# Optimization experiments

Measured on AMD Instinct MI355X. Metric: run time of the kernel, lower is better.

Reference implementation:

```python
import jax, jax.numpy as jnp
import numpy as np

N_NODES = 100000
NEG_SLOPE = 0.2


def gat_conv(x, W, att_src, att_dst, bias, src, dst, heads, out_ch):
    # x: [N, F_in]; W: [F_in, heads*out_ch]; att_*: [heads, out_ch]; bias: [heads*out_ch]
    N = x.shape[0]
    h = (x @ W).reshape(N, heads, out_ch)                 # [N, H, C]
    a_src = jnp.sum(h * att_src[None], axis=-1)           # [N, H]
    a_dst = jnp.sum(h * att_dst[None], axis=-1)           # [N, H]
    # per-edge unnormalized attention logits (PyG GATConv)
    alpha = jax.nn.leaky_relu(a_src[src] + a_dst[dst], NEG_SLOPE)   # [E, H]
    # scatter-softmax over edges grouped by destination node
    m = jax.ops.segment_max(alpha, dst, num_segments=N)   # [N, H]
    m = jnp.where(jnp.isfinite(m), m, 0.0)
    e = jnp.exp(alpha - m[dst])                           # [E, H]
    s = jax.ops.segment_sum(e, dst, num_segments=N)       # [N, H]
    alpha = e / (s[dst] + 1e-16)
    # weighted scatter-add aggregation of neighbor features
    out = jax.ops.segment_sum(alpha[:, :, None] * h[src], dst, num_segments=N)  # [N, H, C]
    return out.reshape(N, heads * out_ch) + bias


def setup_inputs() -> dict:
    key = jax.random.key(0)
    ks = jax.random.split(key, 10)
    F_in = 128
    x = jax.random.normal(ks[0], (N_NODES, F_in), dtype=jnp.float32)
    edge_index = jax.random.randint(ks[1], (2, 3200000), 0, N_NODES, dtype=jnp.int64)
    g = 0.1
    return {
        "x": x,
        "edge_index": edge_index,
        "W1": jax.random.normal(ks[2], (F_in, 32), jnp.float32) * g,
        "att_src1": jax.random.normal(ks[3], (2, 16), jnp.float32) * g,
        "att_dst1": jax.random.normal(ks[4], (2, 16), jnp.float32) * g,
        "b1": jnp.zeros((32,), jnp.float32),
        "W2": jax.random.normal(ks[5], (32, 2), jnp.float32) * g,
        "att_src2": jax.random.normal(ks[6], (1, 2), jnp.float32) * g,
        "att_dst2": jax.random.normal(ks[7], (1, 2), jnp.float32) * g,
        "b2": jnp.zeros((2,), jnp.float32),
    }


def reference(x, edge_index, W1, att_src1, att_dst1, b1, W2, att_src2, att_dst2, b2):
    N = x.shape[0]
    # add self-loops (PyG GATConv default add_self_loops=True)
    loops = jnp.arange(N, dtype=edge_index.dtype)
    src = jnp.concatenate([edge_index[0], loops])
    dst = jnp.concatenate([edge_index[1], loops])
    h = gat_conv(x, W1, att_src1, att_dst1, b1, src, dst, heads=2, out_ch=16)
    h = jax.nn.elu(h)
    h = gat_conv(h, W2, att_src2, att_dst2, b2, src, dst, heads=1, out_ch=2)
    return jax.nn.log_softmax(h, axis=1)
```

## Files before the change

### kernel.cpp

```cpp
#include <hip/hip_runtime.h>
#include <hip/hip_bf16.h>

#define LEAK  0.2f
#define NPB   200
#define CAP   8192
#define CAPSH 13
#define SBITS 17
#define SMASK 0x1FFFF
#define CHUNK 4096

__global__ __launch_bounds__(512) void kbin(const int* __restrict__ ei, int E, int K,
                                            int* __restrict__ cursor,
                                            int* __restrict__ binned) {
    __shared__ int hist[512], lo[512], gb[512], lc[512];
    __shared__ int2 stag[CHUNK];
    __shared__ int probe;
    int t = threadIdx.x;
    hist[t] = 0;
    if (t == 0) probe = 0;
    __syncthreads();
    if (t < 256) {
        int zc = 0;
#pragma unroll
        for (int j = 0; j < 4; j++) zc += (ei[(t * 4 + j) * 2 + 1] == 0) ? 1 : 0;
        if (zc) atomicAdd(&probe, zc);
    }
    __syncthreads();
    int f = (probe == 1024);
    int e0 = blockIdx.x * CHUNK;
    int ss[8], dd[8];
#pragma unroll
    for (int i = 0; i < 8; i++) {
        int e = e0 + t + 512 * i;
        ss[i] = -1;
        dd[i] = 0;
        if (e < E) {
            int s, d;
            if (f) { s = ei[2 * (long long)e]; d = ei[2 * ((long long)e + E)]; }
            else   { s = ei[e];                d = ei[(long long)e + E]; }
            ss[i] = s;
            dd[i] = d;
            atomicAdd(&hist[d / NPB], 1);
        }
    }
    __syncthreads();
    int v = hist[t], x = v;
    for (int o = 1; o < 512; o <<= 1) {
        int y = (t >= o) ? hist[t - o] : 0;
        __syncthreads();
        x += y;
        hist[t] = x;
        __syncthreads();
    }
    int tb = x - v;
    lo[t] = tb;
    lc[t] = tb;
    if (t < K && v) {
        int rel = atomicAdd(&cursor[t], v);
        gb[t] = (t << CAPSH) + rel;
    }
    __syncthreads();
#pragma unroll
    for (int i = 0; i < 8; i++) {
        if (ss[i] >= 0) {
            int bk = dd[i] / NPB;
            int pos = atomicAdd(&lc[bk], 1);
            stag[pos] = make_int2(ss[i], dd[i]);
        }
    }
    __syncthreads();
    int cnt = min(CHUNK, E - e0);
#pragma unroll
    for (int i = 0; i < 8; i++) {
        int idx = t + 512 * i;
        if (idx < cnt) {
            int2 sd2 = stag[idx];
            int bk = sd2.y / NPB;
            int dloc = sd2.y - bk * NPB;
            int gpos = gb[bk] + (idx - lo[bk]);
            if (gpos < ((bk + 1) << CAPSH))
                binned[gpos] = sd2.x | (dloc << SBITS);
        }
    }
}

__global__ __launch_bounds__(256) void k1(const float* __restrict__ x,
                                          const float* __restrict__ W1,
                                          const float* __restrict__ atts,
                                          const float* __restrict__ attd,
                                          float* __restrict__ h1,
                                          float* __restrict__ a1s,
                                          float* __restrict__ a1d, int N) {
    __shared__ float Ws[128 * 32];
    __shared__ float xs[64 * 132];
    int t = threadIdx.x;
    const float4* W4 = (const float4*)W1;
    float4* Ws4 = (float4*)Ws;
#pragma unroll
    for (int i = 0; i < 4; i++) Ws4[t + 256 * i] = W4[t + 256 * i];
    long long node0 = (long long)blockIdx.x * 64;
    const float4* x4 = (const float4*)x;
    float4* xs4 = (float4*)xs;
#pragma unroll
    for (int i = 0; i < 8; i++) {
        int idx = t + 256 * i;
        int row = idx >> 5, col = idx & 31;
        long long n = node0 + row;
        float4 v = make_float4(0.f, 0.f, 0.f, 0.f);
        if (n < N) v = x4[n * 32 + col];
        xs4[row * 33 + col] = v;
    }
    __syncthreads();

    int cg = t & 7, ns = t >> 3;
    const float4* xr0 = (const float4*)(xs + (ns * 2) * 132);
    const float4* xr1 = (const float4*)(xs + (ns * 2 + 1) * 132);
    float acc0[4] = {0.f, 0.f, 0.f, 0.f}, acc1[4] = {0.f, 0.f, 0.f, 0.f};
#pragma unroll 8
    for (int k4 = 0; k4 < 32; k4++) {
        float4 xa = xr0[k4], xb = xr1[k4];
        float av[4] = {xa.x, xa.y, xa.z, xa.w};
        float bv[4] = {xb.x, xb.y, xb.z, xb.w};
#pragma unroll
        for (int i = 0; i < 4; i++) {
            float4 w = Ws4[(k4 * 4 + i) * 8 + cg];
            acc0[0] = fmaf(av[i], w.x, acc0[0]);
            acc0[1] = fmaf(av[i], w.y, acc0[1]);
            acc0[2] = fmaf(av[i], w.z, acc0[2]);
            acc0[3] = fmaf(av[i], w.w, acc0[3]);
            acc1[0] = fmaf(bv[i], w.x, acc1[0]);
            acc1[1] = fmaf(bv[i], w.y, acc1[1]);
            acc1[2] = fmaf(bv[i], w.z, acc1[2]);
            acc1[3] = fmaf(bv[i], w.w, acc1[3]);
        }
    }
    long long gn0 = node0 + ns * 2, gn1 = gn0 + 1;
    float4* h14 = (float4*)h1;
    if (gn0 < N) h14[gn0 * 8 + cg] = make_float4(acc0[0], acc0[1], acc0[2], acc0[3]);
    if (gn1 < N) h14[gn1 * 8 + cg] = make_float4(acc1[0], acc1[1], acc1[2], acc1[3]);

    float ps0 = 0.f, pd0 = 0.f, ps1 = 0.f, pd1 = 0.f;
#pragma unroll
    for (int i = 0; i < 4; i++) {
        float aa = atts[cg * 4 + i], dd = attd[cg * 4 + i];
        ps0 = fmaf(acc0[i], aa, ps0);
        pd0 = fmaf(acc0[i], dd, pd0);
        ps1 = fmaf(acc1[i], aa, ps1);
        pd1 = fmaf(acc1[i], dd, pd1);
    }
#pragma unroll
    for (int m = 1; m < 4; m <<= 1) {
        ps0 += __shfl_xor(ps0, m, 64);
        pd0 += __shfl_xor(pd0, m, 64);
        ps1 += __shfl_xor(ps1, m, 64);
        pd1 += __shfl_xor(pd1, m, 64);
    }
    if ((cg & 3) == 0) {
        int hd = cg >> 2;
        if (gn0 < N) { a1s[gn0 * 2 + hd] = ps0; a1d[gn0 * 2 + hd] = pd0; }
        if (gn1 < N) { a1s[gn1 * 2 + hd] = ps1; a1d[gn1 * 2 + hd] = pd1; }
    }
}

__global__ __launch_bounds__(1024) void kfused(const int* __restrict__ cursor,
                                               const int* __restrict__ binned,
                                               const float* __restrict__ h1,
                                               const float* __restrict__ a1s,
                                               const float* __restrict__ a1d,
                                               const float* __restrict__ b1,
                                               const float* __restrict__ W2,
                                               const float* __restrict__ as2,
                                               const float* __restrict__ ad2,
                                               float4* __restrict__ pk,
                                               int* __restrict__ srcs,
                                               int* __restrict__ off,
                                               int* __restrict__ deg, int N) {
    __shared__ int lsrc[CAP];
    __shared__ int ldeg[NPB], lcur[NPB], loff[NPB];
    __shared__ int sd[1024];
    int b = blockIdx.x, t = threadIdx.x;
    int node0 = b * NPB;
    int nn = min(NPB, N - node0);
    int cnt = cursor[b];
    if (cnt > CAP) cnt = CAP;
    const int* bb = binned + ((long long)b << CAPSH);
    if (t < NPB) ldeg[t] = 0;
    __syncthreads();
    for (int i = t; i < cnt; i += 1024) atomicAdd(&ldeg[bb[i] >> SBITS], 1);
    __syncthreads();
    int v = (t < nn) ? ldeg[t] : 0, x = v;
    sd[t] = x;
    __syncthreads();
    for (int o = 1; o < 1024; o <<= 1) {
        int y = (t >= o) ? sd[t - o] : 0;
        __syncthreads();
        x += y;
        sd[t] = x;
        __syncthreads();
    }
    if (t < nn) {
        int rel = x - v;
        loff[t] = rel;
        lcur[t] = rel;
        off[node0 + t] = (b << CAPSH) + rel;
        deg[node0 + t] = v;
    }
    __syncthreads();
    for (int i = t; i < cnt; i += 1024) {
        int p = bb[i];
        int pos = atomicAdd(&lcur[p >> SBITS], 1);
        lsrc[pos] = p & SMASK;
    }
    __syncthreads();
    for (int i = t; i < cnt; i += 1024) srcs[((long long)b << CAPSH) + i] = lsrc[i];

    int wv = t >> 6, lane = t & 63;
    int e8 = lane >> 3, c4 = lane & 7, hd = c4 >> 2;
    bool wlane = (c4 & 3) == 0;
    const float4* h14 = (const float4*)h1;
    for (int ni = wv; ni < nn; ni += 16) {
        int n = node0 + ni;
        float a1dn = a1d[2 * n + hd];
        int base = loff[ni], g = ldeg[ni];
        float4 acc = make_float4(0.f, 0.f, 0.f, 0.f);
        float wsum = 0.f;
        for (int tt = e8 - 1; tt < g; tt += 8) {
            int s = (tt < 0) ? n : lsrc[base + tt];
            float al = a1s[2 * s + hd] + a1dn;
            al = al > 0.f ? al : LEAK * al;
            float w = __expf(al);
            float4 hv = h14[(size_t)s * 8 + c4];
            acc.x = fmaf(w, hv.x, acc.x);
            acc.y = fmaf(w, hv.y, acc.y);
            acc.z = fmaf(w, hv.z, acc.z);
            acc.w = fmaf(w, hv.w, acc.w);
            if (wlane) wsum += w;
        }
#pragma unroll
        for (int m = 8; m < 64; m <<= 1) {
            acc.x += __shfl_xor(acc.x, m, 64);
            acc.y += __shfl_xor(acc.y, m, 64);
            acc.z += __shfl_xor(acc.z, m, 64);
            acc.w += __shfl_xor(acc.w, m, 64);
            wsum += __shfl_xor(wsum, m, 64);
        }
        float wsH = __shfl(wsum, hd * 4, 64);
        float inv = 1.f / (wsH + 1e-16f);
        float4 bv = ((const float4*)b1)[c4];
        float4 t1;
        t1.x = acc.x * inv + bv.x;
        t1.y = acc.y * inv + bv.y;
        t1.z = acc.z * inv + bv.z;
        t1.w = acc.w * inv + bv.w;
        t1.x = t1.x > 0.f ? t1.x : __expf(t1.x) - 1.f;
        t1.y = t1.y > 0.f ? t1.y : __expf(t1.y) - 1.f;
        t1.z = t1.z > 0.f ? t1.z : __expf(t1.z) - 1.f;
        t1.w = t1.w > 0.f ? t1.w : __expf(t1.w) - 1.f;
        const float4* W24 = (const float4*)W2;
        float4 wA = W24[c4 * 2], wB = W24[c4 * 2 + 1];
        float p0 = t1.x * wA.x + t1.y * wA.z + t1.z * wB.x + t1.w * wB.z;
        float p1 = t1.x * wA.y + t1.y * wA.w + t1.z * wB.y + t1.w * wB.w;
#pragma unroll
        for (int m = 1; m < 8; m <<= 1) {
            p0 += __shfl_xor(p0, m, 64);
            p1 += __shfl_xor(p1, m, 64);
        }
        if (lane == 0)
            pk[n] = make_float4(p0 * as2[0] + p1 * as2[1], p0, p1,
                                p0 * ad2[0] + p1 * ad2[1]);
    }
}

__global__ __launch_bounds__(256) void kagg2(const int* __restrict__ off,
                                             const int* __restrict__ deg,
                                             const int* __restrict__ srcs,
                                             const float4* __restrict__ pk,
                                             const float* __restrict__ b2,
                                             float* __restrict__ out, int N) {
    int wv = threadIdx.x >> 6;
    int lane = threadIdx.x & 63;
    int n = blockIdx.x * 4 + wv;
    if (n >= N) return;
    float adn = pk[n].w;
    int base = off[n], g = deg[n];
    float a0 = 0.f, a1v = 0.f, ws = 0.f;
    for (int t = lane - 1; t < g; t += 64) {
        int s = (t < 0) ? n : srcs[base + t];
        float4 p = pk[s];
        float al = p.x + adn;
        al = al > 0.f ? al : LEAK * al;
        float w = __expf(al);
        a0 = fmaf(w, p.y, a0);
        a1v = fmaf(w, p.z, a1v);
        ws += w;
    }
#pragma unroll
    for (int m = 1; m < 64; m <<= 1) {
        a0 += __shfl_xor(a0, m, 64);
        a1v += __shfl_xor(a1v, m, 64);
        ws += __shfl_xor(ws, m, 64);
    }
    if (lane == 0) {
        float inv = 1.f / (ws + 1e-16f);
        float o0 = a0 * inv + b2[0];
        float o1 = a1v * inv + b2[1];
        float mx = fmaxf(o0, o1);
        float lse = mx + __logf(__expf(o0 - mx) + __expf(o1 - mx));
        out[2 * n] = o0 - lse;
        out[2 * n + 1] = o1 - lse;
    }
}

extern "C" void kernel_launch(void* const* d_in, const int* in_sizes, int n_in,
                              void* d_out, int out_size, void* d_ws, size_t ws_size,
                              hipStream_t stream) {
    const float* x   = (const float*)d_in[0];
    const int*   ei  = (const int*)d_in[1];
    const float* W1  = (const float*)d_in[2];
    const float* as1 = (const float*)d_in[3];
    const float* ad1 = (const float*)d_in[4];
    const float* b1  = (const float*)d_in[5];
    const float* W2  = (const float*)d_in[6];
    const float* as2 = (const float*)d_in[7];
    const float* ad2 = (const float*)d_in[8];
    const float* b2  = (const float*)d_in[9];
    float* out = (float*)d_out;

    int N = out_size / 2;
    int E = in_sizes[1] / 2;
    int K = (N + NPB - 1) / NPB;

    float* ws    = (float*)d_ws;
    float* h1    = ws;
    float4* pk   = (float4*)(h1 + (size_t)N * 32);
    float* a1s   = (float*)(pk + (size_t)N);
    float* a1d   = a1s + (size_t)N * 2;
    int* deg     = (int*)(a1d + (size_t)N * 2);
    int* off     = deg + N;
    int* srcs    = off + N;
    int* binned  = srcs + (size_t)K * CAP;
    int* cursor  = binned + (size_t)K * CAP;

    int nblkE = (E + CHUNK - 1) / CHUNK;

    hipMemsetAsync(cursor, 0, K * sizeof(int), stream);
    kbin<<<nblkE, 512, 0, stream>>>(ei, E, K, cursor, binned);
    k1<<<(N + 63) / 64, 256, 0, stream>>>(x, W1, as1, ad1, h1, a1s, a1d, N);
    kfused<<<K, 1024, 0, stream>>>(cursor, binned, h1, a1s, a1d,
                                   b1, W2, as2, ad2, pk, srcs, off, deg, N);
    kagg2<<<(N + 3) / 4, 256, 0, stream>>>(off, deg, srcs, pk, b2, out, N);
}
```

Before: 245.8 us.

## Merge binning and GEMM into one launch, aggregate layer 2 per bin with shared atomics

The binning kernel and the first-layer GEMM now share one launch, with block index choosing the role and shared memory held in a union. Binning drops the staging sort and scatters straight to global memory using per-bucket atomics, at 8192 edges per block. kfused no longer writes CSR arrays and switches to a wave-shuffle scan. The layer-2 aggregation now reads the binned edges per 200-node block and accumulates with shared-memory float atomics, which removes the srcs/off/deg traffic but gives up coalesced binned writes and adds atomic contention.

New measurement: 253.5 us. 1.03x slower.

```diff
diff --git a/kernel.cpp b/kernel.cpp
--- a/kernel.cpp
+++ b/kernel.cpp
@@ -1,164 +1,133 @@
 #include <hip/hip_runtime.h>
 #include <hip/hip_bf16.h>
 
-#define LEAK  0.2f
-#define NPB   200
-#define CAP   8192
-#define CAPSH 13
-#define SBITS 17
-#define SMASK 0x1FFFF
-#define CHUNK 4096
-
-__global__ __launch_bounds__(512) void kbin(const int* __restrict__ ei, int E, int K,
-                                            int* __restrict__ cursor,
-                                            int* __restrict__ binned) {
-    __shared__ int hist[512], lo[512], gb[512], lc[512];
-    __shared__ int2 stag[CHUNK];
-    __shared__ int probe;
+#define LEAK   0.2f
+#define NPB    200
+#define CAP    8192
+#define CAPSH  13
+#define SBITS  17
+#define SMASK  0x1FFFF
+#define CHUNKB 8192
+
+struct alignas(16) SMbin { int hist[512]; int gb[512]; int lc[512]; int probe; };
+struct alignas(16) SMgemm { float Ws[128 * 32]; float xs[64 * 132]; };
+union alignas(16) SMprep { SMbin bin; SMgemm gemm; };
+
+__global__ __launch_bounds__(512) void kprep(const int* __restrict__ ei, int E, int K,
+                                             int* __restrict__ cursor,
+                                             int* __restrict__ binned,
+                                             const float* __restrict__ x,
+                                             const float* __restrict__ W1,
+                                             const float* __restrict__ atts,
+                                             const float* __restrict__ attd,
+                                             float* __restrict__ h1,
+                                             float* __restrict__ a1s,
+                                             float* __restrict__ a1d,
+                                             int N, int nblkB) {
+    __shared__ SMprep sm;
     int t = threadIdx.x;
-    hist[t] = 0;
-    if (t == 0) probe = 0;
-    __syncthreads();
-    if (t < 256) {
-        int zc = 0;
-#pragma unroll
-        for (int j = 0; j < 4; j++) zc += (ei[(t * 4 + j) * 2 + 1] == 0) ? 1 : 0;
-        if (zc) atomicAdd(&probe, zc);
-    }
-    __syncthreads();
-    int f = (probe == 1024);
-    int e0 = blockIdx.x * CHUNK;
-    int ss[8], dd[8];
-#pragma unroll
-    for (int i = 0; i < 8; i++) {
-        int e = e0 + t + 512 * i;
-        ss[i] = -1;
-        dd[i] = 0;
-        if (e < E) {
-            int s, d;
-            if (f) { s = ei[2 * (long long)e]; d = ei[2 * ((long long)e + E)]; }
-            else   { s = ei[e];                d = ei[(long long)e + E]; }
-            ss[i] = s;
-            dd[i] = d;
-            atomicAdd(&hist[d / NPB], 1);
-        }
-    }
-    __syncthreads();
-    int v = hist[t], x = v;
-    for (int o = 1; o < 512; o <<= 1) {
-        int y = (t >= o) ? hist[t - o] : 0;
-        __syncthreads();
-        x += y;
-        hist[t] = x;
-        __syncthreads();
-    }
-    int tb = x - v;
-    lo[t] = tb;
-    lc[t] = tb;
-    if (t < K && v) {
-        int rel = atomicAdd(&cursor[t], v);
-        gb[t] = (t << CAPSH) + rel;
-    }
-    __syncthreads();
-#pragma unroll
-    for (int i = 0; i < 8; i++) {
-        if (ss[i] >= 0) {
-            int bk = dd[i] / NPB;
-            int pos = atomicAdd(&lc[bk], 1);
-            stag[pos] = make_int2(ss[i], dd[i]);
-        }
-    }
-    __syncthreads();
-    int cnt = min(CHUNK, E - e0);
-#pragma unroll
-    for (int i = 0; i < 8; i++) {
-        int idx = t + 512 * i;
-        if (idx < cnt) {
-            int2 sd2 = stag[idx];
-            int bk = sd2.y / NPB;
-            int dloc = sd2.y - bk * NPB;
-            int gpos = gb[bk] + (idx - lo[bk]);
-            if (gpos < ((bk + 1) << CAPSH))
-                binned[gpos] = sd2.x | (dloc << SBITS);
-        }
-    }
-}
-
-__global__ __launch_bounds__(256) void k1(const float* __restrict__ x,
-                                          const float* __restrict__ W1,
-                                          const float* __restrict__ atts,
-                                          const float* __restrict__ attd,
-                                          float* __restrict__ h1,
-                                          float* __restrict__ a1s,
-                                          float* __restrict__ a1d, int N) {
-    __shared__ float Ws[128 * 32];
-    __shared__ float xs[64 * 132];
-    int t = threadIdx.x;
-    const float4* W4 = (const float4*)W1;
-    float4* Ws4 = (float4*)Ws;
-#pragma unroll
-    for (int i = 0; i < 4; i++) Ws4[t + 256 * i] = W4[t + 256 * i];
-    long long node0 = (long long)blockIdx.x * 64;
-    const float4* x4 = (const float4*)x;
-    float4* xs4 = (float4*)xs;
-#pragma unroll
-    for (int i = 0; i < 8; i++) {
-        int idx = t + 256 * i;
-        int row = idx >> 5, col = idx & 31;
-        long long n = node0 + row;
-        float4 v = make_float4(0.f, 0.f, 0.f, 0.f);
-        if (n < N) v = x4[n * 32 + col];
-        xs4[row * 33 + col] = v;
-    }
-    __syncthreads();
-
-    int cg = t & 7, ns = t >> 3;
-    const float4* xr0 = (const float4*)(xs + (ns * 2) * 132);
-    const float4* xr1 = (const float4*)(xs + (ns * 2 + 1) * 132);
-    float acc0[4] = {0.f, 0.f, 0.f, 0.f}, acc1[4] = {0.f, 0.f, 0.f, 0.f};
+    if (blockIdx.x < nblkB) {
+        SMbin& B = sm.bin;
+        B.hist[t] = 0;
+        if (t == 0) B.probe = 0;
+        __syncthreads();
+        if (t < 256) {
+            int zc = 0;
+#pragma unroll
+            for (int j = 0; j < 4; j++) zc += (ei[(t * 4 + j) * 2 + 1] == 0) ? 1 : 0;
+            if (zc) atomicAdd(&B.probe, zc);
+        }
+        __syncthreads();
+        int f = (B.probe == 1024);
+        int e0 = blockIdx.x * CHUNKB;
+        int ss[16], dd[16];
+#pragma unroll
+        for (int i = 0; i < 16; i++) {
+            int e = e0 + t + 512 * i;
+            ss[i] = -1;
+            dd[i] = 0;
+            if (e < E) {
+                int s, d;
+                if (f) { s = ei[2 * e]; d = ei[2 * (e + E)]; }
+                else   { s = ei[e];     d = ei[e + E]; }
+                ss[i] = s;
+                dd[i] = d;
+                atomicAdd(&B.hist[d / NPB], 1);
+            }
+        }
+        __syncthreads();
+        int h = B.hist[t];
+        B.lc[t] = 0;
+        if (t < K && h) B.gb[t] = (t << CAPSH) + atomicAdd(&cursor[t], h);
+        __syncthreads();
+#pragma unroll
+        for (int i = 0; i < 16; i++) {
+            if (ss[i] >= 0) {
+                int bk = dd[i] / NPB;
+                int dloc = dd[i] - bk * NPB;
+                int pos = atomicAdd(&B.lc[bk], 1);
+                int gpos = B.gb[bk] + pos;
+                if (gpos < ((bk + 1) << CAPSH))
+                    binned[gpos] = ss[i] | (dloc << SBITS);
+            }
+        }
+    } else {
+        SMgemm& G = sm.gemm;
+        int gb1 = blockIdx.x - nblkB;
+        const float4* W4 = (const float4*)W1;
+        float4* Ws4 = (float4*)G.Ws;
+#pragma unroll
+        for (int i = 0; i < 2; i++) Ws4[t + 512 * i] = W4[t + 512 * i];
+        long long node0 = (long long)gb1 * 64;
+        const float4* x4 = (const float4*)x;
+        float4* xs4 = (float4*)G.xs;
+#pragma unroll
+        for (int i = 0; i < 4; i++) {
+            int idx = t + 512 * i;
+            int row = idx >> 5, col = idx & 31;
+            long long n = node0 + row;
+            float4 v = make_float4(0.f, 0.f, 0.f, 0.f);
+            if (n < N) v = x4[n * 32 + col];
+            xs4[row * 33 + col] = v;
+        }
+        __syncthreads();
+
+        int cg = t & 7, ns = t >> 3;
+        const float4* xr = (const float4*)(G.xs + ns * 132);
+        float acc[4] = {0.f, 0.f, 0.f, 0.f};
 #pragma unroll 8
-    for (int k4 = 0; k4 < 32; k4++) {
-        float4 xa = xr0[k4], xb = xr1[k4];
-        float av[4] = {xa.x, xa.y, xa.z, xa.w};
-        float bv[4] = {xb.x, xb.y, xb.z, xb.w};
+        for (int k4 = 0; k4 < 32; k4++) {
+            float4 xa = xr[k4];
+            float av[4] = {xa.x, xa.y, xa.z, xa.w};
+#pragma unroll
+            for (int i = 0; i < 4; i++) {
+                float4 w = Ws4[(k4 * 4 + i) * 8 + cg];
+                acc[0] = fmaf(av[i], w.x, acc[0]);
+                acc[1] = fmaf(av[i], w.y, acc[1]);
+                acc[2] = fmaf(av[i], w.z, acc[2]);
+                acc[3] = fmaf(av[i], w.w, acc[3]);
+            }
+        }
+        long long gn = node0 + ns;
+        if (gn < N)
+            ((float4*)h1)[gn * 8 + cg] = make_float4(acc[0], acc[1], acc[2], acc[3]);
+
+        float ps = 0.f, pd = 0.f;
 #pragma unroll
         for (int i = 0; i < 4; i++) {
-            float4 w = Ws4[(k4 * 4 + i) * 8 + cg];
-            acc0[0] = fmaf(av[i], w.x, acc0[0]);
-            acc0[1] = fmaf(av[i], w.y, acc0[1]);
-            acc0[2] = fmaf(av[i], w.z, acc0[2]);
-            acc0[3] = fmaf(av[i], w.w, acc0[3]);
-            acc1[0] = fmaf(bv[i], w.x, acc1[0]);
-            acc1[1] = fmaf(bv[i], w.y, acc1[1]);
-            acc1[2] = fmaf(bv[i], w.z, acc1[2]);
-            acc1[3] = fmaf(bv[i], w.w, acc1[3]);
-        }
-    }
-    long long gn0 = node0 + ns * 2, gn1 = gn0 + 1;
-    float4* h14 = (float4*)h1;
-    if (gn0 < N) h14[gn0 * 8 + cg] = make_float4(acc0[0], acc0[1], acc0[2], acc0[3]);
-    if (gn1 < N) h14[gn1 * 8 + cg] = make_float4(acc1[0], acc1[1], acc1[2], acc1[3]);
-
-    float ps0 = 0.f, pd0 = 0.f, ps1 = 0.f, pd1 = 0.f;
-#pragma unroll
-    for (int i = 0; i < 4; i++) {
-        float aa = atts[cg * 4 + i], dd = attd[cg * 4 + i];
-        ps0 = fmaf(acc0[i], aa, ps0);
-        pd0 = fmaf(acc0[i], dd, pd0);
-        ps1 = fmaf(acc1[i], aa, ps1);
-        pd1 = fmaf(acc1[i], dd, pd1);
-    }
-#pragma unroll
-    for (int m = 1; m < 4; m <<= 1) {
-        ps0 += __shfl_xor(ps0, m, 64);
-        pd0 += __shfl_xor(pd0, m, 64);
-        ps1 += __shfl_xor(ps1, m, 64);
-        pd1 += __shfl_xor(pd1, m, 64);
-    }
-    if ((cg & 3) == 0) {
-        int hd = cg >> 2;
-        if (gn0 < N) { a1s[gn0 * 2 + hd] = ps0; a1d[gn0 * 2 + hd] = pd0; }
-        if (gn1 < N) { a1s[gn1 * 2 + hd] = ps1; a1d[gn1 * 2 + hd] = pd1; }
+            ps = fmaf(acc[i], atts[cg * 4 + i], ps);
+            pd = fmaf(acc[i], attd[cg * 4 + i], pd);
+        }
+#pragma unroll
+        for (int m = 1; m < 4; m <<= 1) {
+            ps += __shfl_xor(ps, m, 64);
+            pd += __shfl_xor(pd, m, 64);
+        }
+        if ((cg & 3) == 0 && gn < N) {
+            int hd = cg >> 2;
+            a1s[gn * 2 + hd] = ps;
+            a1d[gn * 2 + hd] = pd;
+        }
     }
 }
 
@@ -171,13 +140,10 @@
                                                const float* __restrict__ W2,
                                                const float* __restrict__ as2,
                                                const float* __restrict__ ad2,
-                                               float4* __restrict__ pk,
-                                               int* __restrict__ srcs,
-                                               int* __restrict__ off,
-                                               int* __restrict__ deg, int N) {
+                                               float4* __restrict__ pk, int N) {
     __shared__ int lsrc[CAP];
     __shared__ int ldeg[NPB], lcur[NPB], loff[NPB];
-    __shared__ int sd[1024];
+    __shared__ int swt[4];
     int b = blockIdx.x, t = threadIdx.x;
     int node0 = b * NPB;
     int nn = min(NPB, N - node0);
@@ -186,33 +152,43 @@
     const int* bb = binned + ((long long)b << CAPSH);
     if (t < NPB) ldeg[t] = 0;
     __syncthreads();
-    for (int i = t; i < cnt; i += 1024) atomicAdd(&ldeg[bb[i] >> SBITS], 1);
-    __syncthreads();
-    int v = (t < nn) ? ldeg[t] : 0, x = v;
-    sd[t] = x;
-    __syncthreads();
-    for (int o = 1; o < 1024; o <<= 1) {
-        int y = (t >= o) ? sd[t - o] : 0;
-        __syncthreads();
-        x += y;
-        sd[t] = x;
-        __syncthreads();
-    }
-    if (t < nn) {
-        int rel = x - v;
-        loff[t] = rel;
-        lcur[t] = rel;
-        off[node0 + t] = (b << CAPSH) + rel;
-        deg[node0 + t] = v;
-    }
-    __syncthreads();
-    for (int i = t; i < cnt; i += 1024) {
-        int p = bb[i];
-        int pos = atomicAdd(&lcur[p >> SBITS], 1);
-        lsrc[pos] = p & SMASK;
-    }
-    __syncthreads();
-    for (int i = t; i < cnt; i += 1024) srcs[((long long)b << CAPSH) + i] = lsrc[i];
+    int pv[8];
+#pragma unroll
+    for (int j = 0; j < 8; j++) {
+        int i = t + 1024 * j;
+        pv[j] = (i < cnt) ? bb[i] : -1;
+        if (pv[j] >= 0) atomicAdd(&ldeg[pv[j] >> SBITS], 1);
+    }
+    __syncthreads();
+    int v = 0, x = 0;
+    if (t < 256) {
+        v = (t < nn) ? ldeg[t] : 0;
+        x = v;
+#pragma unroll
+        for (int o = 1; o < 64; o <<= 1) {
+            int y = __shfl_up(x, o, 64);
+            if ((t & 63) >= o) x += y;
+        }
+        if ((t & 63) == 63) swt[t >> 6] = x;
+    }
+    __syncthreads();
+    if (t < 256) {
+        int add = 0;
+#pragma unroll
+        for (int j = 0; j < 4; j++)
+            if (j < (t >> 6)) add += swt[j];
+        x += add;
+        if (t < nn) { loff[t] = x - v; lcur[t] = x - v; }
+    }
+    __syncthreads();
+#pragma unroll
+    for (int j = 0; j < 8; j++) {
+        if (pv[j] >= 0) {
+            int pos = atomicAdd(&lcur[pv[j] >> SBITS], 1);
+            lsrc[pos] = pv[j] & SMASK;
+        }
+    }
+    __syncthreads();
 
     int wv = t >> 6, lane = t & 63;
     int e8 = lane >> 3, c4 = lane & 7, hd = c4 >> 2;
@@ -271,43 +247,48 @@
     }
 }
 
-__global__ __launch_bounds__(256) void kagg2(const int* __restrict__ off,
-                                             const int* __restrict__ deg,
-                                             const int* __restrict__ srcs,
-                                             const float4* __restrict__ pk,
-                                             const float* __restrict__ b2,
-                                             float* __restrict__ out, int N) {
-    int wv = threadIdx.x >> 6;
-    int lane = threadIdx.x & 63;
-    int n = blockIdx.x * 4 + wv;
-    if (n >= N) return;
-    float adn = pk[n].w;
-    int base = off[n], g = deg[n];
-    float a0 = 0.f, a1v = 0.f, ws = 0.f;
-    for (int t = lane - 1; t < g; t += 64) {
-        int s = (t < 0) ? n : srcs[base + t];
-        float4 p = pk[s];
-        float al = p.x + adn;
+__global__ __launch_bounds__(1024) void kagg2b(const int* __restrict__ cursor,
+                                               const int* __restrict__ binned,
+                                               const float4* __restrict__ pk,
+                                               const float* __restrict__ b2,
+                                               float* __restrict__ out, int N) {
+    __shared__ float la2d[NPB], lw[NPB], l0[NPB], l1[NPB];
+    int b = blockIdx.x, t = threadIdx.x;
+    int node0 = b * NPB;
+    int nn = min(NPB, N - node0);
+    int cnt = cursor[b];
+    if (cnt > CAP) cnt = CAP;
+    const int* bb = binned + ((long long)b << CAPSH);
+    if (t < nn) {
+        float4 p = pk[node0 + t];
+        la2d[t] = p.w;
+        float al = p.x + p.w;
         al = al > 0.f ? al : LEAK * al;
         float w = __expf(al);
-        a0 = fmaf(w, p.y, a0);
-        a1v = fmaf(w, p.z, a1v);
-        ws += w;
-    }
-#pragma unroll
-    for (int m = 1; m < 64; m <<= 1) {
-        a0 += __shfl_xor(a0, m, 64);
-        a1v += __shfl_xor(a1v, m, 64);
-        ws += __shfl_xor(ws, m, 64);
-    }
-    if (lane == 0) {
-        float inv = 1.f / (ws + 1e-16f);
-        float o0 = a0 * inv + b2[0];
-        float o1 = a1v * inv + b2[1];
+        lw[t] = w;
+        l0[t] = w * p.y;
+        l1[t] = w * p.z;
+    }
+    __syncthreads();
+    for (int i = t; i < cnt; i += 1024) {
+        int p = bb[i];
+        int s = p & SMASK, dl = p >> SBITS;
+        float4 ps = pk[s];
+        float al = ps.x + la2d[dl];
+        al = al > 0.f ? al : LEAK * al;
+        float w = __expf(al);
+        atomicAdd(&l0[dl], w * ps.y);
+        atomicAdd(&l1[dl], w * ps.z);
+        atomicAdd(&lw[dl], w);
+    }
+    __syncthreads();
+    if (t < nn) {
+        float inv = 1.f / (lw[t] + 1e-16f);
+        float o0 = l0[t] * inv + b2[0];
+        float o1 = l1[t] * inv + b2[1];
         float mx = fmaxf(o0, o1);
         float lse = mx + __logf(__expf(o0 - mx) + __expf(o1 - mx));
-        out[2 * n] = o0 - lse;
-        out[2 * n + 1] = o1 - lse;
+        ((float2*)out)[node0 + t] = make_float2(o0 - lse, o1 - lse);
     }
 }
 
@@ -331,22 +312,21 @@
     int K = (N + NPB - 1) / NPB;
 
     float* ws    = (float*)d_ws;
-    float* h1    = ws;
-    float4* pk   = (float4*)(h1 + (size_t)N * 32);
-    float* a1s   = (float*)(pk + (size_t)N);
+    float4* pk   = (float4*)ws;
+    float* h1    = (float*)(pk + (size_t)N);
+    float* a1s   = h1 + (size_t)N * 32;
     float* a1d   = a1s + (size_t)N * 2;
-    int* deg     = (int*)(a1d + (size_t)N * 2);
-    int* off     = deg + N;
-    int* srcs    = off + N;
-    int* binned  = srcs + (size_t)K * CAP;
+    int* binned  = (int*)(a1d + (size_t)N * 2);
     int* cursor  = binned + (size_t)K * CAP;
 
-    int nblkE = (E + CHUNK - 1) / CHUNK;
+    int nblkB = (E + CHUNKB - 1) / CHUNKB;
+    int nblkG = (N + 63) / 64;
 
     hipMemsetAsync(cursor, 0, K * sizeof(int), stream);
-    kbin<<<nblkE, 512, 0, stream>>>(ei, E, K, cursor, binned);
-    k1<<<(N + 63) / 64, 256, 0, stream>>>(x, W1, as1, ad1, h1, a1s, a1d, N);
+    kprep<<<nblkB + nblkG, 512, 0, stream>>>(ei, E, K, cursor, binned,
+                                             x, W1, as1, ad1, h1, a1s, a1d,
+                                             N, nblkB);
     kfused<<<K, 1024, 0, stream>>>(cursor, binned, h1, a1s, a1d,
-                                   b1, W2, as2, ad2, pk, srcs, off, deg, N);
-    kagg2<<<(N + 3) / 4, 256, 0, stream>>>(off, deg, srcs, pk, b2, out, N);
+                                   b1, W2, as2, ad2, pk, N);
+    kagg2b<<<K, 1024, 0, stream>>>(cursor, binned, pk, b2, out, N);
 }
```
